# Kernel tuning notes

Measured on AMD Instinct MI355X. Metric: run time of the kernel, lower is better.

Reference implementation:

```python
import jax, jax.numpy as jnp
import numpy as np

EPS = 1e-5


def setup_inputs() -> dict:
    key = jax.random.key(0)
    k1, k2, k3 = jax.random.split(key, 3)
    B, C, H, W = 64, 512, 28, 28
    G = 8
    x = jax.random.normal(k1, (B, C, H, W), dtype=jnp.float32)
    weight = jax.random.normal(k2, (G,), dtype=jnp.float32)
    bias = jax.random.normal(k3, (G,), dtype=jnp.float32)
    return {"x": x, "weight": weight, "bias": bias, "groups": G}


def reference(x, weight, bias, groups):
    B, C, H, W = x.shape
    G = groups
    cpg = C // G
    hw = H * W
    xg = x.reshape(B, G, cpg, hw)                       # [B,G,cpg,HW]
    # per-channel spatial mean
    means = jnp.mean(xg, axis=-1, keepdims=True)        # [B,G,cpg,1]
    # similarity map: dot product of each spatial vector with channel-mean vector
    s = jnp.sum(xg * means, axis=2)                     # [B,G,HW]
    # normalize s over spatial dim (population variance, eps=1e-5)
    mu = jnp.mean(s, axis=-1, keepdims=True)
    var = jnp.mean(jnp.square(s - mu), axis=-1, keepdims=True)
    t = (s - mu) * jax.lax.rsqrt(var + EPS)             # [B,G,HW]
    gate = jax.nn.sigmoid(t * weight[None, :, None] + bias[None, :, None])
    out = xg * gate[:, :, None, :]                      # broadcast gate over channels
    return out.reshape(B, C, H, W)
```

## Files before the change

### kernel.cpp

```cpp
#include <hip/hip_runtime.h>


#define HW    784
#define HW4   196
#define CPG   64
#define NG    8
#define K4    12
#define TAIL4 4

__global__ __launch_bounds__(1024, 4)
void sge_kernel(const float* __restrict__ x,
                const float* __restrict__ weight,
                const float* __restrict__ bias,
                float* __restrict__ out) {
    __shared__ float sbuf[16 * HW];
    __shared__ float redbuf[32];

    const int t    = threadIdx.x;
    const int c    = t >> 4;
    const int j    = t & 15;
    const int wave = t >> 6;
    const int lane = t & 63;

    const int bg = blockIdx.x;
    const int g  = bg & (NG - 1);
    const size_t base4 = (size_t)bg * (CPG * HW4) + (size_t)c * HW4;

    const float4* xp = (const float4*)x + base4;
    float4 v[K4 + 1];
#pragma unroll
    for (int k = 0; k < K4; ++k) v[k] = xp[j + 16 * k];
    v[K4] = (j < TAIL4) ? xp[192 + j] : make_float4(0.f, 0.f, 0.f, 0.f);
#pragma unroll
    for (int k = 0; k <= K4; ++k)
        asm volatile("" : "+v"(v[k].x), "+v"(v[k].y), "+v"(v[k].z), "+v"(v[k].w));

    float cs = 0.f;
#pragma unroll
    for (int k = 0; k <= K4; ++k) cs += (v[k].x + v[k].y) + (v[k].z + v[k].w);
    cs += __shfl_xor(cs, 1, 64);
    cs += __shfl_xor(cs, 2, 64);
    cs += __shfl_xor(cs, 4, 64);
    cs += __shfl_xor(cs, 8, 64);
    const float mean_c = cs * (1.0f / (float)HW);

    float4* srow = (float4*)(sbuf + wave * HW);
#pragma unroll
    for (int k = 0; k <= K4; ++k) {
        float4 w;
        w.x = v[k].x * mean_c; w.y = v[k].y * mean_c;
        w.z = v[k].z * mean_c; w.w = v[k].w * mean_c;
        w.x += __shfl_xor(w.x, 16, 64); w.x += __shfl_xor(w.x, 32, 64);
        w.y += __shfl_xor(w.y, 16, 64); w.y += __shfl_xor(w.y, 32, 64);
        w.z += __shfl_xor(w.z, 16, 64); w.z += __shfl_xor(w.z, 32, 64);
        w.w += __shfl_xor(w.w, 16, 64); w.w += __shfl_xor(w.w, 32, 64);
        if (k < K4) {
            if (lane < 16) srow[j + 16 * k] = w;
        } else {
            if (lane < TAIL4) srow[192 + j] = w;
        }
    }
    __syncthreads();

    float s = 0.f;
    if (t < HW) {
#pragma unroll
        for (int w = 0; w < 16; ++w) s += sbuf[w * HW + t];
    }

    float rs = s, rs2 = s * s;
#pragma unroll
    for (int m = 1; m < 64; m <<= 1) {
        rs  += __shfl_xor(rs,  m, 64);
        rs2 += __shfl_xor(rs2, m, 64);
    }
    if (lane == 0) { redbuf[wave] = rs; redbuf[16 + wave] = rs2; }
    __syncthreads();

    float sum_s = 0.f, sum_s2 = 0.f;
#pragma unroll
    for (int w = 0; w < 16; ++w) { sum_s += redbuf[w]; sum_s2 += redbuf[16 + w]; }
    const float mu   = sum_s * (1.0f / (float)HW);
    const float var  = sum_s2 * (1.0f / (float)HW) - mu * mu;
    const float rstd = rsqrtf(var + 1e-5f);

    const float wg  = weight[g];
    const float bgv = bias[g];
    if (t < HW) {
        const float z = (s - mu) * rstd * wg + bgv;
        sbuf[t] = 1.0f / (1.0f + __expf(-z));
    }
    __syncthreads();

    const float4* gate4 = (const float4*)sbuf;
    float4* op = (float4*)out + base4;
#pragma unroll
    for (int k = 0; k < K4; ++k) {
        const float4 gv = gate4[j + 16 * k];
        float4 o;
        o.x = v[k].x * gv.x; o.y = v[k].y * gv.y;
        o.z = v[k].z * gv.z; o.w = v[k].w * gv.w;
        op[j + 16 * k] = o;
    }
    if (j < TAIL4) {
        const float4 gv = gate4[192 + j];
        float4 o;
        o.x = v[K4].x * gv.x; o.y = v[K4].y * gv.y;
        o.z = v[K4].z * gv.z; o.w = v[K4].w * gv.w;
        op[192 + j] = o;
    }
}

extern "C" void kernel_launch(void* const* d_in, const int* in_sizes, int n_in,
                              void* d_out, int out_size, void* d_ws, size_t ws_size,
                              hipStream_t stream) {
    const float* x      = (const float*)d_in[0];
    const float* weight = (const float*)d_in[1];
    const float* bias   = (const float*)d_in[2];
    float* out = (float*)d_out;
    sge_kernel<<<dim3(512), dim3(1024), 0, stream>>>(x, weight, bias, out);
}
```

Measured before the change: 195.3 us.

## Use 256-thread blocks with 4 threads per channel holding whole rows in registers

Shrinks each block from 1024 to 256 threads. Each group of 4 threads now owns one channel and keeps all 49 float4s of it in registers, so the padded tail handling goes away and fewer shuffles are needed. The spatial partial sums are written to 16 shared rows and each thread then reduces 3-4 spatial positions. The cost is much higher register pressure per thread (196 floats) and fewer, wider per-thread memory streams with stride-4 float4 access, which may hurt coalescing and occupancy.

Measured after the change: 190.4 us. -2.5%, faster.

```diff
diff --git a/kernel.cpp b/kernel.cpp
--- a/kernel.cpp
+++ b/kernel.cpp
@@ -3,92 +3,96 @@
 
 #define HW    784
 #define HW4   196
-#define CPG   64
 #define NG    8
-#define K4    12
-#define TAIL4 4
+#define K4    49
 
-__global__ __launch_bounds__(1024, 4)
+__global__ __launch_bounds__(256, 2)
 void sge_kernel(const float* __restrict__ x,
                 const float* __restrict__ weight,
                 const float* __restrict__ bias,
                 float* __restrict__ out) {
     __shared__ float sbuf[16 * HW];
-    __shared__ float redbuf[32];
+    __shared__ float redbuf[8];
 
     const int t    = threadIdx.x;
-    const int c    = t >> 4;
-    const int j    = t & 15;
+    const int lane = t & 63;
     const int wave = t >> 6;
-    const int lane = t & 63;
+    const int j    = t & 3;
 
     const int bg = blockIdx.x;
     const int g  = bg & (NG - 1);
-    const size_t base4 = (size_t)bg * (CPG * HW4) + (size_t)c * HW4;
+    const size_t base4 = (size_t)bg * (64 * HW4) + (size_t)(t >> 2) * HW4;
 
     const float4* xp = (const float4*)x + base4;
-    float4 v[K4 + 1];
+    float4 v[K4];
 #pragma unroll
-    for (int k = 0; k < K4; ++k) v[k] = xp[j + 16 * k];
-    v[K4] = (j < TAIL4) ? xp[192 + j] : make_float4(0.f, 0.f, 0.f, 0.f);
+    for (int k = 0; k < K4; ++k) v[k] = xp[j + 4 * k];
 #pragma unroll
-    for (int k = 0; k <= K4; ++k)
+    for (int k = 0; k < K4; ++k)
         asm volatile("" : "+v"(v[k].x), "+v"(v[k].y), "+v"(v[k].z), "+v"(v[k].w));
 
     float cs = 0.f;
 #pragma unroll
-    for (int k = 0; k <= K4; ++k) cs += (v[k].x + v[k].y) + (v[k].z + v[k].w);
+    for (int k = 0; k < K4; ++k) cs += (v[k].x + v[k].y) + (v[k].z + v[k].w);
     cs += __shfl_xor(cs, 1, 64);
     cs += __shfl_xor(cs, 2, 64);
-    cs += __shfl_xor(cs, 4, 64);
-    cs += __shfl_xor(cs, 8, 64);
     const float mean_c = cs * (1.0f / (float)HW);
 
-    float4* srow = (float4*)(sbuf + wave * HW);
+    const int  row    = (wave << 2) + (lane >> 4);
+    float4*    srow   = (float4*)(sbuf + row * HW);
+    const bool writer = ((lane >> 2) & 3) == 0;
 #pragma unroll
-    for (int k = 0; k <= K4; ++k) {
+    for (int k = 0; k < K4; ++k) {
         float4 w;
         w.x = v[k].x * mean_c; w.y = v[k].y * mean_c;
         w.z = v[k].z * mean_c; w.w = v[k].w * mean_c;
-        w.x += __shfl_xor(w.x, 16, 64); w.x += __shfl_xor(w.x, 32, 64);
-        w.y += __shfl_xor(w.y, 16, 64); w.y += __shfl_xor(w.y, 32, 64);
-        w.z += __shfl_xor(w.z, 16, 64); w.z += __shfl_xor(w.z, 32, 64);
-        w.w += __shfl_xor(w.w, 16, 64); w.w += __shfl_xor(w.w, 32, 64);
-        if (k < K4) {
-            if (lane < 16) srow[j + 16 * k] = w;
-        } else {
-            if (lane < TAIL4) srow[192 + j] = w;
-        }
+        w.x += __shfl_xor(w.x, 4, 64);  w.x += __shfl_xor(w.x, 8, 64);
+        w.y += __shfl_xor(w.y, 4, 64);  w.y += __shfl_xor(w.y, 8, 64);
+        w.z += __shfl_xor(w.z, 4, 64);  w.z += __shfl_xor(w.z, 8, 64);
+        w.w += __shfl_xor(w.w, 4, 64);  w.w += __shfl_xor(w.w, 8, 64);
+        if (writer) srow[j + 4 * k] = w;
     }
     __syncthreads();
 
-    float s = 0.f;
-    if (t < HW) {
+    float s0 = 0.f, s1 = 0.f, s2 = 0.f, s3 = 0.f;
 #pragma unroll
-        for (int w = 0; w < 16; ++w) s += sbuf[w * HW + t];
+    for (int r = 0; r < 16; ++r) {
+        const float* rw = sbuf + r * HW;
+        s0 += rw[t];
+        s1 += rw[t + 256];
+        s2 += rw[t + 512];
+        if (t < 16) s3 += rw[t + 768];
     }
 
-    float rs = s, rs2 = s * s;
+    float rs  = s0 + s1 + s2 + s3;
+    float rs2 = s0 * s0 + s1 * s1 + s2 * s2 + s3 * s3;
 #pragma unroll
     for (int m = 1; m < 64; m <<= 1) {
         rs  += __shfl_xor(rs,  m, 64);
         rs2 += __shfl_xor(rs2, m, 64);
     }
-    if (lane == 0) { redbuf[wave] = rs; redbuf[16 + wave] = rs2; }
+    if (lane == 0) { redbuf[wave] = rs; redbuf[4 + wave] = rs2; }
     __syncthreads();
 
-    float sum_s = 0.f, sum_s2 = 0.f;
-#pragma unroll
-    for (int w = 0; w < 16; ++w) { sum_s += redbuf[w]; sum_s2 += redbuf[16 + w]; }
+    const float sum_s  = redbuf[0] + redbuf[1] + redbuf[2] + redbuf[3];
+    const float sum_s2 = redbuf[4] + redbuf[5] + redbuf[6] + redbuf[7];
     const float mu   = sum_s * (1.0f / (float)HW);
     const float var  = sum_s2 * (1.0f / (float)HW) - mu * mu;
     const float rstd = rsqrtf(var + 1e-5f);
+    const float wg   = weight[g];
+    const float bgv  = bias[g];
 
-    const float wg  = weight[g];
-    const float bgv = bias[g];
-    if (t < HW) {
-        const float z = (s - mu) * rstd * wg + bgv;
-        sbuf[t] = 1.0f / (1.0f + __expf(-z));
+    {
+        const float z0 = (s0 - mu) * rstd * wg + bgv;
+        const float z1 = (s1 - mu) * rstd * wg + bgv;
+        const float z2 = (s2 - mu) * rstd * wg + bgv;
+        sbuf[t]       = 1.0f / (1.0f + __expf(-z0));
+        sbuf[t + 256] = 1.0f / (1.0f + __expf(-z1));
+        sbuf[t + 512] = 1.0f / (1.0f + __expf(-z2));
+        if (t < 16) {
+            const float z3 = (s3 - mu) * rstd * wg + bgv;
+            sbuf[t + 768] = 1.0f / (1.0f + __expf(-z3));
+        }
     }
     __syncthreads();
 
@@ -96,18 +100,11 @@
     float4* op = (float4*)out + base4;
 #pragma unroll
     for (int k = 0; k < K4; ++k) {
-        const float4 gv = gate4[j + 16 * k];
+        const float4 gv = gate4[j + 4 * k];
         float4 o;
         o.x = v[k].x * gv.x; o.y = v[k].y * gv.y;
         o.z = v[k].z * gv.z; o.w = v[k].w * gv.w;
-        op[j + 16 * k] = o;
-    }
-    if (j < TAIL4) {
-        const float4 gv = gate4[192 + j];
-        float4 o;
-        o.x = v[K4].x * gv.x; o.y = v[K4].y * gv.y;
-        o.z = v[K4].z * gv.z; o.w = v[K4].w * gv.w;
-        op[192 + j] = o;
+        op[j + 4 * k] = o;
     }
 }
 
@@ -118,5 +115,5 @@
     const float* weight = (const float*)d_in[1];
     const float* bias   = (const float*)d_in[2];
     float* out = (float*)d_out;
-    sge_kernel<<<dim3(512), dim3(1024), 0, stream>>>(x, weight, bias, out);
+    sge_kernel<<<dim3(512), dim3(256), 0, stream>>>(x, weight, bias, out);
 }
```
